# Kernel optimization log

Hardware: AMD Instinct MI355X
Metric: run time of the kernel (lower is better)

Reference implementation:

```python
import jax, jax.numpy as jnp
import numpy as np
import math

D_MODEL = 1024
NUM_HEADS = 16
D_K = D_MODEL // NUM_HEADS
B, S = 2, 2048


def setup_inputs() -> dict:
    key = jax.random.key(0)
    ks = jax.random.split(key, 11)
    scale = 1.0 / math.sqrt(D_MODEL)
    inp = {
        "query": jax.random.normal(ks[0], (B, S, D_MODEL), jnp.float32),
        "key": jax.random.normal(ks[1], (B, S, D_MODEL), jnp.float32),
        "value": jax.random.normal(ks[2], (B, S, D_MODEL), jnp.float32),
        "Wq": jax.random.normal(ks[3], (D_MODEL, D_MODEL), jnp.float32) * scale,
        "bq": jnp.zeros((D_MODEL,), jnp.float32),
        "Wk": jax.random.normal(ks[4], (D_MODEL, D_MODEL), jnp.float32) * scale,
        "bk": jnp.zeros((D_MODEL,), jnp.float32),
        "Wv": jax.random.normal(ks[5], (D_MODEL, D_MODEL), jnp.float32) * scale,
        "bv": jnp.zeros((D_MODEL,), jnp.float32),
        "Wo": jax.random.normal(ks[6], (D_MODEL, D_MODEL), jnp.float32) * scale,
        "bo": jnp.zeros((D_MODEL,), jnp.float32),
    }
    return inp


def reference(query, key, value, Wq, bq, Wk, bk, Wv, bv, Wo, bo):
    b, s, _ = query.shape
    # QKV projections (torch Linear: x @ W.T + b)
    Q = query @ Wq.T + bq
    K = key @ Wk.T + bk
    V = value @ Wv.T + bv
    # [b, h, s, d_k]
    Q = Q.reshape(b, s, NUM_HEADS, D_K).transpose(0, 2, 1, 3)
    K = K.reshape(b, s, NUM_HEADS, D_K).transpose(0, 2, 1, 3)
    V = V.reshape(b, s, NUM_HEADS, D_K).transpose(0, 2, 1, 3)
    score = jnp.einsum("bhqd,bhkd->bhqk", Q, K) / math.sqrt(D_K)
    attn = jax.nn.softmax(score, axis=-1)
    out = jnp.einsum("bhqk,bhkd->bhqd", attn, V)
    out = out.transpose(0, 2, 1, 3).reshape(b, s, D_MODEL)
    return out @ Wo.T + bo
```

## Files before the change

kernel.cpp:

```cpp
#include <hip/hip_runtime.h>

#define NHEADS 16
#define SEQ    2048
#define BATCH  2
#define DMODEL 1024
#define MTOT   4096

typedef __attribute__((ext_vector_type(8)))  short short8;
typedef __attribute__((ext_vector_type(4)))  float f32x4;
typedef __attribute__((ext_vector_type(16))) float f32x16;

__device__ __forceinline__ unsigned short f32_to_bf16_rn(float x) {
  unsigned int u = __float_as_uint(x);
  u += 0x7fffu + ((u >> 16) & 1u);
  return (unsigned short)(u >> 16);
}

__device__ __forceinline__ unsigned cvt_pk_bf16(float lo, float hi_) {
  unsigned r;
  asm("v_cvt_pk_bf16_f32 %0, %1, %2" : "=v"(r) : "v"(lo), "v"(hi_));
  return r;
}

__device__ __forceinline__ void permlane32_swap(unsigned &a, unsigned &b) {
  asm("v_permlane32_swap_b32 %0, %1" : "+v"(a), "+v"(b));
}

__device__ __forceinline__ void async16(void* lds, const void* g) {
  __builtin_amdgcn_global_load_lds((const __attribute__((address_space(1))) unsigned int*)g,
                                   (__attribute__((address_space(3))) unsigned int*)lds, 16, 0, 0);
}

__global__ void cvt_w_kernel(const float* __restrict__ w0, const float* __restrict__ w1,
                             const float* __restrict__ w2, const float* __restrict__ w3,
                             unsigned short* __restrict__ obase)
{
  const int which = blockIdx.y;
  const float* src = which==0 ? w0 : which==1 ? w1 : which==2 ? w2 : w3;
  const int i = (blockIdx.x*256 + threadIdx.x)*8;
  const float4 v0 = *(const float4*)(src + i);
  const float4 v1 = *(const float4*)(src + i + 4);
  union { unsigned short u[8]; uint4 v; } r;
  r.u[0] = f32_to_bf16_rn(v0.x); r.u[1] = f32_to_bf16_rn(v0.y);
  r.u[2] = f32_to_bf16_rn(v0.z); r.u[3] = f32_to_bf16_rn(v0.w);
  r.u[4] = f32_to_bf16_rn(v1.x); r.u[5] = f32_to_bf16_rn(v1.y);
  r.u[6] = f32_to_bf16_rn(v1.z); r.u[7] = f32_to_bf16_rn(v1.w);
  *(uint4*)(obase + (size_t)which*1048576 + i) = r.v;
}

template<int BM>
__device__ __forceinline__ void gemm_core(const unsigned short* __restrict__ A,
                                          const unsigned short* __restrict__ W,
                                          unsigned short* sA, unsigned short* sB,
                                          int m0, int n0, f32x4 (&acc)[BM/32][4])
{
  constexpr int MI = BM/32;
  const int t = threadIdx.x;
  const int lane = t & 63;
  const int wv = t >> 6;
  const int wm = wv >> 1, wn = wv & 1;
  const int lr = lane & 15, lk = lane >> 4;

  for (int kt = 0; kt < DMODEL/64; ++kt) {
    #pragma unroll
    for (int g = 0; g < MI; ++g) {
      const int o  = g*4096 + t*16;
      const int so = o ^ (((o >> 7) & 7) << 4);
      const int row = so >> 7, colE = (so & 127) >> 1;
      async16((char*)sA + o, A + (size_t)(m0 + row)*DMODEL + kt*64 + colE);
    }
    #pragma unroll
    for (int g = 0; g < 4; ++g) {
      const int o  = g*4096 + t*16;
      const int so = o ^ (((o >> 7) & 7) << 4);
      const int row = so >> 7, colE = (so & 127) >> 1;
      async16((char*)sB + o, W + (size_t)(n0 + row)*DMODEL + kt*64 + colE);
    }
    __syncthreads();
    #pragma unroll
    for (int ks = 0; ks < 2; ++ks) {
      short8 af[MI], bf[4];
      #pragma unroll
      for (int mi = 0; mi < MI; ++mi) {
        const int row = wm*(BM/2) + mi*16 + lr;
        const int sl  = (ks*4 + lk) ^ (row & 7);
        af[mi] = *(const short8*)(sA + row*64 + sl*8);
      }
      #pragma unroll
      for (int ni = 0; ni < 4; ++ni) {
        const int row = wn*64 + ni*16 + lr;
        const int sl  = (ks*4 + lk) ^ (row & 7);
        bf[ni] = *(const short8*)(sB + row*64 + sl*8);
      }
      #pragma unroll
      for (int mi = 0; mi < MI; ++mi)
        #pragma unroll
        for (int ni = 0; ni < 4; ++ni)
          acc[mi][ni] = __builtin_amdgcn_mfma_f32_16x16x32_bf16(af[mi], bf[ni], acc[mi][ni], 0, 0, 0);
    }
    __syncthreads();
  }
}

__global__ __launch_bounds__(256, 3)
void qkv_gemm_kernel(const float* __restrict__ Xq, const float* __restrict__ Xk,
                     const float* __restrict__ Xv,
                     const unsigned short* __restrict__ Wq, const unsigned short* __restrict__ Wk,
                     const unsigned short* __restrict__ Wv,
                     const float* __restrict__ bq, const float* __restrict__ bk,
                     const float* __restrict__ bv,
                     unsigned short* __restrict__ Qp, unsigned short* __restrict__ Kp,
                     unsigned short* __restrict__ Vtp)
{
  constexpr int MI = 4;
  constexpr int NK = DMODEL/64;
  __shared__ __align__(16) unsigned short smem[24576];
  unsigned short* sA = smem;

  const int m0   = blockIdx.x * 128;
  const int nabs = blockIdx.y * 128;
  const int wsel = nabs >> 10;
  const int n0   = nabs & 1023;
  const float* A          = wsel==0 ? Xq : wsel==1 ? Xk : Xv;
  const unsigned short* W = wsel==0 ? Wq : wsel==1 ? Wk : Wv;
  const float* bias       = wsel==0 ? bq : wsel==1 ? bk : bv;

  const int t = threadIdx.x, lane = t & 63, wvx = t >> 6;
  const int wm = wvx >> 1, wn = wvx & 1;
  const int lr = lane & 15, lk = lane >> 4;

  int aRow[MI], aCol[MI], aO[MI];
  #pragma unroll
  for (int g = 0; g < MI; ++g) {
    const int o  = g*4096 + t*16;
    const int so = o ^ (((o >> 7) & 7) << 4);
    aO[g] = o; aRow[g] = so >> 7; aCol[g] = (so & 127) >> 1;
  }

  f32x4 acc[MI][4];
  #pragma unroll
  for (int mi = 0; mi < MI; ++mi)
    #pragma unroll
    for (int ni = 0; ni < 4; ++ni)
      acc[mi][ni] = {0.f, 0.f, 0.f, 0.f};

  float4 aLo[MI], aHi[MI];
  #pragma unroll
  for (int g = 0; g < MI; ++g) {
    const float* s = A + (size_t)(m0 + aRow[g])*DMODEL + aCol[g];
    aLo[g] = *(const float4*)(s);
    aHi[g] = *(const float4*)(s + 4);
  }
  #pragma unroll
  for (int g = 0; g < 4; ++g)
    async16((char*)smem + 16384 + aO[g], W + (size_t)(n0 + aRow[g])*DMODEL + aCol[g]);

  for (int kt = 0; kt < NK; ++kt) {
    asm volatile("s_waitcnt vmcnt(0)" ::: "memory");
    #pragma unroll
    for (int g = 0; g < MI; ++g) {
      union { uint4 v; unsigned u[4]; } r;
      r.u[0] = cvt_pk_bf16(aLo[g].x, aLo[g].y);
      r.u[1] = cvt_pk_bf16(aLo[g].z, aLo[g].w);
      r.u[2] = cvt_pk_bf16(aHi[g].x, aHi[g].y);
      r.u[3] = cvt_pk_bf16(aHi[g].z, aHi[g].w);
      *(uint4*)((char*)sA + aO[g]) = r.v;
    }
    asm volatile("s_waitcnt lgkmcnt(0)" ::: "memory");
    __builtin_amdgcn_s_barrier();
    if (kt + 1 < NK) {
      #pragma unroll
      for (int g = 0; g < MI; ++g) {
        const float* s = A + (size_t)(m0 + aRow[g])*DMODEL + (kt + 1)*64 + aCol[g];
        aLo[g] = *(const float4*)(s);
        aHi[g] = *(const float4*)(s + 4);
      }
      const int nb = 16384 + ((kt + 1) & 1)*8192*2;
      #pragma unroll
      for (int g = 0; g < 4; ++g)
        async16((char*)smem + nb + aO[g], W + (size_t)(n0 + aRow[g])*DMODEL + (kt + 1)*64 + aCol[g]);
    }
    const unsigned short* sB = smem + 8192 + (kt & 1)*8192;
    #pragma unroll
    for (int ks = 0; ks < 2; ++ks) {
      short8 af[MI], bf[4];
      #pragma unroll
      for (int mi = 0; mi < MI; ++mi) {
        const int row = wm*64 + mi*16 + lr;
        const int sl  = (ks*4 + lk) ^ (row & 7);
        af[mi] = *(const short8*)(sA + row*64 + sl*8);
      }
      #pragma unroll
      for (int ni = 0; ni < 4; ++ni) {
        const int row = wn*64 + ni*16 + lr;
        const int sl  = (ks*4 + lk) ^ (row & 7);
        bf[ni] = *(const short8*)(sB + row*64 + sl*8);
      }
      #pragma unroll
      for (int mi = 0; mi < MI; ++mi)
        #pragma unroll
        for (int ni = 0; ni < 4; ++ni)
          acc[mi][ni] = __builtin_amdgcn_mfma_f32_16x16x32_bf16(af[mi], bf[ni], acc[mi][ni], 0, 0, 0);
    }
    __builtin_amdgcn_s_barrier();
  }
  __syncthreads();

  if (wsel == 2) {
    #pragma unroll
    for (int ni = 0; ni < 4; ++ni) {
      const float badd = bias[n0 + wn*64 + ni*16 + lr];
      #pragma unroll
      for (int mi = 0; mi < MI; ++mi)
        #pragma unroll
        for (int r = 0; r < 4; ++r) {
          const int ml = wm*64 + mi*16 + lk*4 + r;
          smem[(wn*64 + ni*16 + lr)*132 + ml] = f32_to_bf16_rn(acc[mi][ni][r] + badd);
        }
    }
    __syncthreads();
    const int bb = m0 >> 11, s0 = m0 & 2047;
    const int jr = (t & 15)*8, nr = t >> 4;
    #pragma unroll
    for (int pass = 0; pass < 8; ++pass) {
      const int n  = pass*16 + nr;
      const int nn = n0 + n, hh = nn >> 6, d = nn & 63;
      const short8 v = *(const short8*)(smem + n*132 + jr);
      *(short8*)(Vtp + (((size_t)bb*NHEADS + hh)*64 + d)*SEQ + s0 + jr) = v;
    }
  } else {
    unsigned short* dst = wsel==0 ? Qp : Kp;
    const float qscale = (wsel == 0) ? 0.125f * 1.4426950408889634f : 1.0f;
    #pragma unroll
    for (int ni = 0; ni < 4; ++ni) {
      const int nn = n0 + wn*64 + ni*16 + lr;
      const float badd = bias[nn];
      const int hh = nn >> 6, d = nn & 63;
      #pragma unroll
      for (int mi = 0; mi < MI; ++mi) {
        #pragma unroll
        for (int r = 0; r < 4; ++r) {
          const int m = m0 + wm*64 + mi*16 + lk*4 + r;
          const int bb = m >> 11, s = m & 2047;
          const float v = (acc[mi][ni][r] + badd) * qscale;
          dst[(((size_t)bb*NHEADS + hh)*SEQ + s)*64 + d] = f32_to_bf16_rn(v);
        }
      }
    }
  }
}

__global__ __launch_bounds__(256, 2)
void attn_kernel(const unsigned short* __restrict__ Qp, const unsigned short* __restrict__ Kp,
                 const unsigned short* __restrict__ Vtp, unsigned short* __restrict__ Op)
{
  __shared__ __align__(16) unsigned short sm[16384];
  constexpr int NT = SEQ/64;

  const int t = threadIdx.x, lane = t & 63, w = t >> 6;
  const int lq = lane & 31, hi = lane >> 5;
  const int f   = blockIdx.x;
  const int wid = (f & 7)*64 + (f >> 3);
  const int qt = wid & 15, h = (wid >> 4) & 15, b = wid >> 8;

  const size_t bh = (size_t)b*NHEADS + h;
  const unsigned short* Qh = Qp  + bh*SEQ*64;
  const unsigned short* Kh = Kp  + bh*SEQ*64;
  const unsigned short* Vh = Vtp + bh*64*SEQ;
  const int q0 = qt*128 + w*32;

  short8 qf[4];
  #pragma unroll
  for (int ks = 0; ks < 4; ++ks)
    qf[ks] = *(const short8*)(Qh + (size_t)(q0 + lq)*64 + ks*16 + hi*8);

  f32x16 z16;
  #pragma unroll
  for (int r = 0; r < 16; ++r) z16[r] = 0.f;

  const unsigned short* srcp0;
  size_t sstride;
  if (w < 2) { srcp0 = Kh + (size_t)(w*32 + lq)*64 + hi*8;       sstride = 64*64; }
  else       { srcp0 = Vh + (size_t)((w-2)*32 + lq)*2048 + hi*8; sstride = 64;    }

  #pragma unroll
  for (int i = 0; i < 4; ++i)
    async16((char*)sm + w*4096 + i*1024, srcp0 + i*16);

  f32x16 o[2];
  float lsa[4] = {0.f, 0.f, 0.f, 0.f};
  #pragma unroll
  for (int d = 0; d < 2; ++d)
    #pragma unroll
    for (int r = 0; r < 16; ++r) o[d][r] = 0.f;

  for (int kt = 0; kt < NT; ++kt) {
    {
      const unsigned short* sp = srcp0 + (size_t)((kt + 1) & (NT - 1))*sstride;
      const int nb = ((kt + 1) & 1) * 16384;
      #pragma unroll
      for (int i = 0; i < 4; ++i)
        async16((char*)sm + nb + w*4096 + i*1024, sp + i*16);
    }
    asm volatile("s_waitcnt vmcnt(4)" ::: "memory");
    __builtin_amdgcn_s_barrier();

    const unsigned short* base  = sm + (kt & 1)*8192;
    const unsigned short* vbase = base + 4096;

    f32x16 st[2];
    #pragma unroll
    for (int sub = 0; sub < 2; ++sub) {
      #pragma unroll
      for (int ks = 0; ks < 4; ++ks) {
        const short8 kf = *(const short8*)(base + (sub*4 + ks)*512 + lane*8);
        if (ks == 0)
          st[sub] = __builtin_amdgcn_mfma_f32_32x32x16_bf16(kf, qf[0], z16, 0, 0, 0);
        else
          st[sub] = __builtin_amdgcn_mfma_f32_32x32x16_bf16(kf, qf[ks], st[sub], 0, 0, 0);
      }
    }

    unsigned pw[2][8];
    #pragma unroll
    for (int sub = 0; sub < 2; ++sub) {
      #pragma unroll
      for (int r = 0; r < 16; ++r) {
        const float p = __builtin_amdgcn_exp2f(st[sub][r]);
        st[sub][r] = p;
        lsa[r & 3] += p;
      }
      unsigned x0 = cvt_pk_bf16(st[sub][0],  st[sub][1]);
      unsigned x1 = cvt_pk_bf16(st[sub][2],  st[sub][3]);
      unsigned y0 = cvt_pk_bf16(st[sub][4],  st[sub][5]);
      unsigned y1 = cvt_pk_bf16(st[sub][6],  st[sub][7]);
      permlane32_swap(x0, y0);
      permlane32_swap(x1, y1);
      pw[sub][0] = x0; pw[sub][1] = x1; pw[sub][2] = y0; pw[sub][3] = y1;
      unsigned z0 = cvt_pk_bf16(st[sub][8],  st[sub][9]);
      unsigned z1 = cvt_pk_bf16(st[sub][10], st[sub][11]);
      unsigned w0 = cvt_pk_bf16(st[sub][12], st[sub][13]);
      unsigned w1 = cvt_pk_bf16(st[sub][14], st[sub][15]);
      permlane32_swap(z0, w0);
      permlane32_swap(z1, w1);
      pw[sub][4] = z0; pw[sub][5] = z1; pw[sub][6] = w0; pw[sub][7] = w1;
    }

    #pragma unroll
    for (int sub = 0; sub < 2; ++sub) {
      const short8 v00 = *(const short8*)(vbase + (0*4 + 2*sub    )*512 + lane*8);
      const short8 v01 = *(const short8*)(vbase + (0*4 + 2*sub + 1)*512 + lane*8);
      const short8 v10 = *(const short8*)(vbase + (1*4 + 2*sub    )*512 + lane*8);
      const short8 v11 = *(const short8*)(vbase + (1*4 + 2*sub + 1)*512 + lane*8);
      union { unsigned u[4]; short8 s; } pA, pB;
      pA.u[0] = pw[sub][0]; pA.u[1] = pw[sub][1]; pA.u[2] = pw[sub][2]; pA.u[3] = pw[sub][3];
      pB.u[0] = pw[sub][4]; pB.u[1] = pw[sub][5]; pB.u[2] = pw[sub][6]; pB.u[3] = pw[sub][7];
      o[0] = __builtin_amdgcn_mfma_f32_32x32x16_bf16(v00, pA.s, o[0], 0, 0, 0);
      o[1] = __builtin_amdgcn_mfma_f32_32x32x16_bf16(v10, pA.s, o[1], 0, 0, 0);
      o[0] = __builtin_amdgcn_mfma_f32_32x32x16_bf16(v01, pB.s, o[0], 0, 0, 0);
      o[1] = __builtin_amdgcn_mfma_f32_32x32x16_bf16(v11, pB.s, o[1], 0, 0, 0);
    }
    asm volatile("" ::: "memory");
    __builtin_amdgcn_s_barrier();
  }

  float lsum = (lsa[0] + lsa[1]) + (lsa[2] + lsa[3]);
  lsum += __shfl_xor(lsum, 32);
  const float inv = __builtin_amdgcn_rcpf(lsum);
  unsigned short* orow = Op + ((size_t)b*SEQ + q0 + lq)*DMODEL + h*64;
  #pragma unroll
  for (int dblk = 0; dblk < 2; ++dblk)
    #pragma unroll
    for (int g = 0; g < 4; ++g) {
      union { unsigned short us[4]; uint2 v; } pk;
      #pragma unroll
      for (int r = 0; r < 4; ++r) pk.us[r] = f32_to_bf16_rn(o[dblk][g*4 + r] * inv);
      *(uint2*)(orow + dblk*32 + g*8 + hi*4) = pk.v;
    }
}

__global__ __launch_bounds__(256, 2)
void oproj_gemm_kernel(const unsigned short* __restrict__ Oin, const unsigned short* __restrict__ Wo,
                       const float* __restrict__ bo, float* __restrict__ out)
{
  constexpr int BM = 64;
  constexpr int MI = BM/32;
  __shared__ __align__(16) unsigned short sA[BM*64];
  __shared__ __align__(16) unsigned short sB[128*64];
  const int m0 = blockIdx.x * BM;
  const int n0 = blockIdx.y * 128;

  f32x4 acc[MI][4];
  #pragma unroll
  for (int mi = 0; mi < MI; ++mi)
    #pragma unroll
    for (int ni = 0; ni < 4; ++ni)
      acc[mi][ni] = {0.f,0.f,0.f,0.f};

  gemm_core<BM>(Oin, Wo, sA, sB, m0, n0, acc);

  const int t = threadIdx.x, lane = t & 63, wvx = t >> 6;
  const int wm = wvx >> 1, wn = wvx & 1;
  const int lr = lane & 15, lk = lane >> 4;

  #pragma unroll
  for (int ni = 0; ni < 4; ++ni) {
    const int nn = n0 + wn*64 + ni*16 + lr;
    const float badd = bo[nn];
    #pragma unroll
    for (int mi = 0; mi < MI; ++mi)
      #pragma unroll
      for (int r = 0; r < 4; ++r) {
        const int m = m0 + wm*(BM/2) + mi*16 + lk*4 + r;
        out[(size_t)m*DMODEL + nn] = acc[mi][ni][r] + badd;
      }
  }
}

extern "C" void kernel_launch(void* const* d_in, const int* in_sizes, int n_in,
                              void* d_out, int out_size, void* d_ws, size_t ws_size,
                              hipStream_t stream) {
  const float* query = (const float*)d_in[0];
  const float* key   = (const float*)d_in[1];
  const float* value = (const float*)d_in[2];
  const float* Wq    = (const float*)d_in[3];
  const float* bq    = (const float*)d_in[4];
  const float* Wk    = (const float*)d_in[5];
  const float* bk    = (const float*)d_in[6];
  const float* Wv    = (const float*)d_in[7];
  const float* bv    = (const float*)d_in[8];
  const float* Wo    = (const float*)d_in[9];
  const float* bo    = (const float*)d_in[10];

  const size_t NX = (size_t)MTOT*DMODEL;
  const size_t NW = (size_t)DMODEL*DMODEL;
  unsigned short* w   = (unsigned short*)d_ws;
  unsigned short* Wqp = w + 3*NX;
  unsigned short* Wkp = Wqp + NW;
  unsigned short* Wvp = Wkp + NW;
  unsigned short* Wop = Wvp + NW;
  unsigned short* Qp  = Wop + NW;
  unsigned short* Kp  = Qp  + NX;
  unsigned short* Vtp = Kp  + NX;
  unsigned short* Opb = Vtp + NX;

  cvt_w_kernel<<<dim3(512, 4), 256, 0, stream>>>(Wq, Wk, Wv, Wo, Wqp);
  qkv_gemm_kernel<<<dim3(32, 24), 256, 0, stream>>>(
      query, key, value, Wqp, Wkp, Wvp, bq, bk, bv, Qp, Kp, Vtp);
  attn_kernel<<<dim3(512), 256, 0, stream>>>(Qp, Kp, Vtp, Opb);
  oproj_gemm_kernel<<<dim3(64, 8), 256, 0, stream>>>(Opb, Wop, bo, (float*)d_out);
}
```

Baseline: 105.0 us.

## Deepen A-operand register prefetch to two stages with partial vmcnt waits

```diff
diff --git a/kernel.cpp b/kernel.cpp
--- a/kernel.cpp
+++ b/kernel.cpp
@@ -144,41 +144,52 @@
     for (int ni = 0; ni < 4; ++ni)
       acc[mi][ni] = {0.f, 0.f, 0.f, 0.f};
 
-  float4 aLo[MI], aHi[MI];
+  float4 aLoA[MI], aHiA[MI], aLoB[MI], aHiB[MI];
+
   #pragma unroll
   for (int g = 0; g < MI; ++g) {
     const float* s = A + (size_t)(m0 + aRow[g])*DMODEL + aCol[g];
-    aLo[g] = *(const float4*)(s);
-    aHi[g] = *(const float4*)(s + 4);
+    aLoA[g] = *(const float4*)(s);
+    aHiA[g] = *(const float4*)(s + 4);
   }
   #pragma unroll
   for (int g = 0; g < 4; ++g)
     async16((char*)smem + 16384 + aO[g], W + (size_t)(n0 + aRow[g])*DMODEL + aCol[g]);
-
-  for (int kt = 0; kt < NK; ++kt) {
-    asm volatile("s_waitcnt vmcnt(0)" ::: "memory");
+  #pragma unroll
+  for (int g = 0; g < MI; ++g) {
+    const float* s = A + (size_t)(m0 + aRow[g])*DMODEL + 64 + aCol[g];
+    aLoB[g] = *(const float4*)(s);
+    aHiB[g] = *(const float4*)(s + 4);
+  }
+
+  auto body = [&](int kt, float4 (&lo)[MI], float4 (&hi)[MI]) {
+    {
+      const int bkt = (kt + 1) & (NK - 1);
+      const int nb  = 16384 + ((kt + 1) & 1)*16384;
+      #pragma unroll
+      for (int g = 0; g < 4; ++g)
+        async16((char*)smem + nb + aO[g], W + (size_t)(n0 + aRow[g])*DMODEL + bkt*64 + aCol[g]);
+    }
+    asm volatile("s_waitcnt vmcnt(12)" ::: "memory");
     #pragma unroll
     for (int g = 0; g < MI; ++g) {
       union { uint4 v; unsigned u[4]; } r;
-      r.u[0] = cvt_pk_bf16(aLo[g].x, aLo[g].y);
-      r.u[1] = cvt_pk_bf16(aLo[g].z, aLo[g].w);
-      r.u[2] = cvt_pk_bf16(aHi[g].x, aHi[g].y);
-      r.u[3] = cvt_pk_bf16(aHi[g].z, aHi[g].w);
+      r.u[0] = cvt_pk_bf16(lo[g].x, lo[g].y);
+      r.u[1] = cvt_pk_bf16(lo[g].z, lo[g].w);
+      r.u[2] = cvt_pk_bf16(hi[g].x, hi[g].y);
+      r.u[3] = cvt_pk_bf16(hi[g].z, hi[g].w);
       *(uint4*)((char*)sA + aO[g]) = r.v;
     }
     asm volatile("s_waitcnt lgkmcnt(0)" ::: "memory");
     __builtin_amdgcn_s_barrier();
-    if (kt + 1 < NK) {
+    {
+      const int akt = (kt + 2) & (NK - 1);
       #pragma unroll
       for (int g = 0; g < MI; ++g) {
-        const float* s = A + (size_t)(m0 + aRow[g])*DMODEL + (kt + 1)*64 + aCol[g];
-        aLo[g] = *(const float4*)(s);
-        aHi[g] = *(const float4*)(s + 4);
-      }
-      const int nb = 16384 + ((kt + 1) & 1)*8192*2;
-      #pragma unroll
-      for (int g = 0; g < 4; ++g)
-        async16((char*)smem + nb + aO[g], W + (size_t)(n0 + aRow[g])*DMODEL + (kt + 1)*64 + aCol[g]);
+        const float* s = A + (size_t)(m0 + aRow[g])*DMODEL + akt*64 + aCol[g];
+        lo[g] = *(const float4*)(s);
+        hi[g] = *(const float4*)(s + 4);
+      }
     }
     const unsigned short* sB = smem + 8192 + (kt & 1)*8192;
     #pragma unroll
@@ -203,6 +214,11 @@
           acc[mi][ni] = __builtin_amdgcn_mfma_f32_16x16x32_bf16(af[mi], bf[ni], acc[mi][ni], 0, 0, 0);
     }
     __builtin_amdgcn_s_barrier();
+  };
+
+  for (int kt = 0; kt < NK; kt += 2) {
+    body(kt,     aLoA, aHiA);
+    body(kt + 1, aLoB, aHiB);
   }
   __syncthreads();
 
```

New measurement: 112.7 us. +7.3%, slower.

## Double attention KV tile to 128 keys and pin scheduling with sched barriers

Applied to the files above, without the earlier changes.

```diff
diff --git a/kernel.cpp b/kernel.cpp
--- a/kernel.cpp
+++ b/kernel.cpp
@@ -168,6 +168,7 @@
     }
     asm volatile("s_waitcnt lgkmcnt(0)" ::: "memory");
     __builtin_amdgcn_s_barrier();
+    __builtin_amdgcn_sched_barrier(0);
     if (kt + 1 < NK) {
       #pragma unroll
       for (int g = 0; g < MI; ++g) {
@@ -202,7 +203,9 @@
         for (int ni = 0; ni < 4; ++ni)
           acc[mi][ni] = __builtin_amdgcn_mfma_f32_16x16x32_bf16(af[mi], bf[ni], acc[mi][ni], 0, 0, 0);
     }
+    asm volatile("" ::: "memory");
     __builtin_amdgcn_s_barrier();
+    __builtin_amdgcn_sched_barrier(0);
   }
   __syncthreads();
 
@@ -254,8 +257,8 @@
 void attn_kernel(const unsigned short* __restrict__ Qp, const unsigned short* __restrict__ Kp,
                  const unsigned short* __restrict__ Vtp, unsigned short* __restrict__ Op)
 {
-  __shared__ __align__(16) unsigned short sm[16384];
-  constexpr int NT = SEQ/64;
+  __shared__ __align__(16) unsigned short sm[32768];
+  constexpr int NT = SEQ/128;
 
   const int t = threadIdx.x, lane = t & 63, w = t >> 6;
   const int lq = lane & 31, hi = lane >> 5;
@@ -280,12 +283,22 @@
 
   const unsigned short* srcp0;
   size_t sstride;
-  if (w < 2) { srcp0 = Kh + (size_t)(w*32 + lq)*64 + hi*8;       sstride = 64*64; }
-  else       { srcp0 = Vh + (size_t)((w-2)*32 + lq)*2048 + hi*8; sstride = 64;    }
-
-  #pragma unroll
-  for (int i = 0; i < 4; ++i)
-    async16((char*)sm + w*4096 + i*1024, srcp0 + i*16);
+  int offi[8];
+  if (w < 2) {
+    srcp0 = Kh + (size_t)(w*64 + lq)*64 + hi*8;
+    sstride = 128*64;
+    #pragma unroll
+    for (int i = 0; i < 8; ++i) offi[i] = (i >> 2)*2048 + (i & 3)*16;
+  } else {
+    srcp0 = Vh + (size_t)((w - 2)*32 + lq)*2048 + hi*8;
+    sstride = 128;
+    #pragma unroll
+    for (int i = 0; i < 8; ++i) offi[i] = i*16;
+  }
+
+  #pragma unroll
+  for (int i = 0; i < 8; ++i)
+    async16((char*)sm + w*8192 + i*1024, srcp0 + offi[i]);
 
   f32x16 o[2];
   float lsa[4] = {0.f, 0.f, 0.f, 0.f};
@@ -297,64 +310,57 @@
   for (int kt = 0; kt < NT; ++kt) {
     {
       const unsigned short* sp = srcp0 + (size_t)((kt + 1) & (NT - 1))*sstride;
-      const int nb = ((kt + 1) & 1) * 16384;
-      #pragma unroll
-      for (int i = 0; i < 4; ++i)
-        async16((char*)sm + nb + w*4096 + i*1024, sp + i*16);
-    }
-    asm volatile("s_waitcnt vmcnt(4)" ::: "memory");
+      const int nb = ((kt + 1) & 1) * 32768;
+      #pragma unroll
+      for (int i = 0; i < 8; ++i)
+        async16((char*)sm + nb + w*8192 + i*1024, sp + offi[i]);
+    }
+    asm volatile("s_waitcnt vmcnt(8)" ::: "memory");
     __builtin_amdgcn_s_barrier();
-
-    const unsigned short* base  = sm + (kt & 1)*8192;
-    const unsigned short* vbase = base + 4096;
-
-    f32x16 st[2];
-    #pragma unroll
-    for (int sub = 0; sub < 2; ++sub) {
+    __builtin_amdgcn_sched_barrier(0);
+    asm volatile("" ::: "memory");
+
+    const unsigned short* kb = sm + (kt & 1)*16384;
+    const unsigned short* vb = kb + 8192;
+
+    #pragma unroll
+    for (int sub = 0; sub < 4; ++sub) {
+      f32x16 st;
       #pragma unroll
       for (int ks = 0; ks < 4; ++ks) {
-        const short8 kf = *(const short8*)(base + (sub*4 + ks)*512 + lane*8);
+        const short8 kf = *(const short8*)(kb + (sub*4 + ks)*512 + lane*8);
         if (ks == 0)
-          st[sub] = __builtin_amdgcn_mfma_f32_32x32x16_bf16(kf, qf[0], z16, 0, 0, 0);
+          st = __builtin_amdgcn_mfma_f32_32x32x16_bf16(kf, qf[0], z16, 0, 0, 0);
         else
-          st[sub] = __builtin_amdgcn_mfma_f32_32x32x16_bf16(kf, qf[ks], st[sub], 0, 0, 0);
-      }
-    }
-
-    unsigned pw[2][8];
-    #pragma unroll
-    for (int sub = 0; sub < 2; ++sub) {
+          st = __builtin_amdgcn_mfma_f32_32x32x16_bf16(kf, qf[ks], st, 0, 0, 0);
+      }
       #pragma unroll
       for (int r = 0; r < 16; ++r) {
-        const float p = __builtin_amdgcn_exp2f(st[sub][r]);
-        st[sub][r] = p;
+        const float p = __builtin_amdgcn_exp2f(st[r]);
+        st[r] = p;
         lsa[r & 3] += p;
       }
-      unsigned x0 = cvt_pk_bf16(st[sub][0],  st[sub][1]);
-      unsigned x1 = cvt_pk_bf16(st[sub][2],  st[sub][3]);
-      unsigned y0 = cvt_pk_bf16(st[sub][4],  st[sub][5]);
-      unsigned y1 = cvt_pk_bf16(st[sub][6],  st[sub][7]);
-      permlane32_swap(x0, y0);
-      permlane32_swap(x1, y1);
-      pw[sub][0] = x0; pw[sub][1] = x1; pw[sub][2] = y0; pw[sub][3] = y1;
-      unsigned z0 = cvt_pk_bf16(st[sub][8],  st[sub][9]);
-      unsigned z1 = cvt_pk_bf16(st[sub][10], st[sub][11]);
-      unsigned w0 = cvt_pk_bf16(st[sub][12], st[sub][13]);
-      unsigned w1 = cvt_pk_bf16(st[sub][14], st[sub][15]);
-      permlane32_swap(z0, w0);
-      permlane32_swap(z1, w1);
-      pw[sub][4] = z0; pw[sub][5] = z1; pw[sub][6] = w0; pw[sub][7] = w1;
-    }
-
-    #pragma unroll
-    for (int sub = 0; sub < 2; ++sub) {
-      const short8 v00 = *(const short8*)(vbase + (0*4 + 2*sub    )*512 + lane*8);
-      const short8 v01 = *(const short8*)(vbase + (0*4 + 2*sub + 1)*512 + lane*8);
-      const short8 v10 = *(const short8*)(vbase + (1*4 + 2*sub    )*512 + lane*8);
-      const short8 v11 = *(const short8*)(vbase + (1*4 + 2*sub + 1)*512 + lane*8);
       union { unsigned u[4]; short8 s; } pA, pB;
-      pA.u[0] = pw[sub][0]; pA.u[1] = pw[sub][1]; pA.u[2] = pw[sub][2]; pA.u[3] = pw[sub][3];
-      pB.u[0] = pw[sub][4]; pB.u[1] = pw[sub][5]; pB.u[2] = pw[sub][6]; pB.u[3] = pw[sub][7];
+      {
+        unsigned x0 = cvt_pk_bf16(st[0],  st[1]);
+        unsigned x1 = cvt_pk_bf16(st[2],  st[3]);
+        unsigned y0 = cvt_pk_bf16(st[4],  st[5]);
+        unsigned y1 = cvt_pk_bf16(st[6],  st[7]);
+        permlane32_swap(x0, y0);
+        permlane32_swap(x1, y1);
+        pA.u[0] = x0; pA.u[1] = x1; pA.u[2] = y0; pA.u[3] = y1;
+        unsigned z0 = cvt_pk_bf16(st[8],  st[9]);
+        unsigned z1 = cvt_pk_bf16(st[10], st[11]);
+        unsigned w0 = cvt_pk_bf16(st[12], st[13]);
+        unsigned w1 = cvt_pk_bf16(st[14], st[15]);
+        permlane32_swap(z0, w0);
+        permlane32_swap(z1, w1);
+        pB.u[0] = z0; pB.u[1] = z1; pB.u[2] = w0; pB.u[3] = w1;
+      }
+      const short8 v00 = *(const short8*)(vb + (0*8 + 2*sub    )*512 + lane*8);
+      const short8 v01 = *(const short8*)(vb + (0*8 + 2*sub + 1)*512 + lane*8);
+      const short8 v10 = *(const short8*)(vb + (1*8 + 2*sub    )*512 + lane*8);
+      const short8 v11 = *(const short8*)(vb + (1*8 + 2*sub + 1)*512 + lane*8);
       o[0] = __builtin_amdgcn_mfma_f32_32x32x16_bf16(v00, pA.s, o[0], 0, 0, 0);
       o[1] = __builtin_amdgcn_mfma_f32_32x32x16_bf16(v10, pA.s, o[1], 0, 0, 0);
       o[0] = __builtin_amdgcn_mfma_f32_32x32x16_bf16(v01, pB.s, o[0], 0, 0, 0);
@@ -362,7 +368,9 @@
     }
     asm volatile("" ::: "memory");
     __builtin_amdgcn_s_barrier();
-  }
+    __builtin_amdgcn_sched_barrier(0);
+  }
+  asm volatile("s_waitcnt vmcnt(0)" ::: "memory");
 
   float lsum = (lsa[0] + lsa[1]) + (lsa[2] + lsa[3]);
   lsum += __shfl_xor(lsum, 32);
```

Result: slower. 107.2 us (+2.1%).

## Enlarge QKV GEMM block tile to 256x128 with 512 threads

Applied to the files above, without the earlier changes.

```diff
diff --git a/kernel.cpp b/kernel.cpp
--- a/kernel.cpp
+++ b/kernel.cpp
@@ -102,7 +102,7 @@
   }
 }
 
-__global__ __launch_bounds__(256, 3)
+__global__ __launch_bounds__(512, 2)
 void qkv_gemm_kernel(const float* __restrict__ Xq, const float* __restrict__ Xk,
                      const float* __restrict__ Xv,
                      const unsigned short* __restrict__ Wq, const unsigned short* __restrict__ Wk,
@@ -114,10 +114,9 @@
 {
   constexpr int MI = 4;
   constexpr int NK = DMODEL/64;
-  __shared__ __align__(16) unsigned short smem[24576];
-  unsigned short* sA = smem;
-
-  const int m0   = blockIdx.x * 128;
+  __shared__ __align__(16) unsigned short smem[33792];
+
+  const int m0   = blockIdx.x * 256;
   const int nabs = blockIdx.y * 128;
   const int wsel = nabs >> 10;
   const int n0   = nabs & 1023;
@@ -129,13 +128,20 @@
   const int wm = wvx >> 1, wn = wvx & 1;
   const int lr = lane & 15, lk = lane >> 4;
 
-  int aRow[MI], aCol[MI], aO[MI];
-  #pragma unroll
-  for (int g = 0; g < MI; ++g) {
-    const int o  = g*4096 + t*16;
+  int aRow[4], aCol[4], aO[4];
+  #pragma unroll
+  for (int g = 0; g < 4; ++g) {
+    const int o  = g*8192 + t*16;
     const int so = o ^ (((o >> 7) & 7) << 4);
     aO[g] = o; aRow[g] = so >> 7; aCol[g] = (so & 127) >> 1;
   }
+  int bRow[2], bCol[2], bO[2];
+  #pragma unroll
+  for (int g = 0; g < 2; ++g) {
+    const int o  = g*8192 + t*16;
+    const int so = o ^ (((o >> 7) & 7) << 4);
+    bO[g] = o; bRow[g] = so >> 7; bCol[g] = (so & 127) >> 1;
+  }
 
   f32x4 acc[MI][4];
   #pragma unroll
@@ -144,43 +150,43 @@
     for (int ni = 0; ni < 4; ++ni)
       acc[mi][ni] = {0.f, 0.f, 0.f, 0.f};
 
-  float4 aLo[MI], aHi[MI];
-  #pragma unroll
-  for (int g = 0; g < MI; ++g) {
+  float4 aLo[4], aHi[4];
+  #pragma unroll
+  for (int g = 0; g < 4; ++g) {
     const float* s = A + (size_t)(m0 + aRow[g])*DMODEL + aCol[g];
     aLo[g] = *(const float4*)(s);
     aHi[g] = *(const float4*)(s + 4);
   }
   #pragma unroll
-  for (int g = 0; g < 4; ++g)
-    async16((char*)smem + 16384 + aO[g], W + (size_t)(n0 + aRow[g])*DMODEL + aCol[g]);
+  for (int g = 0; g < 2; ++g)
+    async16((char*)smem + 32768 + bO[g], W + (size_t)(n0 + bRow[g])*DMODEL + bCol[g]);
 
   for (int kt = 0; kt < NK; ++kt) {
     asm volatile("s_waitcnt vmcnt(0)" ::: "memory");
     #pragma unroll
-    for (int g = 0; g < MI; ++g) {
+    for (int g = 0; g < 4; ++g) {
       union { uint4 v; unsigned u[4]; } r;
       r.u[0] = cvt_pk_bf16(aLo[g].x, aLo[g].y);
       r.u[1] = cvt_pk_bf16(aLo[g].z, aLo[g].w);
       r.u[2] = cvt_pk_bf16(aHi[g].x, aHi[g].y);
       r.u[3] = cvt_pk_bf16(aHi[g].z, aHi[g].w);
-      *(uint4*)((char*)sA + aO[g]) = r.v;
+      *(uint4*)((char*)smem + aO[g]) = r.v;
     }
     asm volatile("s_waitcnt lgkmcnt(0)" ::: "memory");
     __builtin_amdgcn_s_barrier();
     if (kt + 1 < NK) {
       #pragma unroll
-      for (int g = 0; g < MI; ++g) {
+      for (int g = 0; g < 4; ++g) {
         const float* s = A + (size_t)(m0 + aRow[g])*DMODEL + (kt + 1)*64 + aCol[g];
         aLo[g] = *(const float4*)(s);
         aHi[g] = *(const float4*)(s + 4);
       }
-      const int nb = 16384 + ((kt + 1) & 1)*8192*2;
-      #pragma unroll
-      for (int g = 0; g < 4; ++g)
-        async16((char*)smem + nb + aO[g], W + (size_t)(n0 + aRow[g])*DMODEL + (kt + 1)*64 + aCol[g]);
-    }
-    const unsigned short* sB = smem + 8192 + (kt & 1)*8192;
+      const int nb = 32768 + ((kt + 1) & 1)*16384;
+      #pragma unroll
+      for (int g = 0; g < 2; ++g)
+        async16((char*)smem + nb + bO[g], W + (size_t)(n0 + bRow[g])*DMODEL + (kt + 1)*64 + bCol[g]);
+    }
+    const unsigned short* sBu = smem + 16384 + (kt & 1)*8192;
     #pragma unroll
     for (int ks = 0; ks < 2; ++ks) {
       short8 af[MI], bf[4];
@@ -188,13 +194,13 @@
       for (int mi = 0; mi < MI; ++mi) {
         const int row = wm*64 + mi*16 + lr;
         const int sl  = (ks*4 + lk) ^ (row & 7);
-        af[mi] = *(const short8*)(sA + row*64 + sl*8);
+        af[mi] = *(const short8*)(smem + row*64 + sl*8);
       }
       #pragma unroll
       for (int ni = 0; ni < 4; ++ni) {
         const int row = wn*64 + ni*16 + lr;
         const int sl  = (ks*4 + lk) ^ (row & 7);
-        bf[ni] = *(const short8*)(sB + row*64 + sl*8);
+        bf[ni] = *(const short8*)(sBu + row*64 + sl*8);
       }
       #pragma unroll
       for (int mi = 0; mi < MI; ++mi)
@@ -215,17 +221,17 @@
         #pragma unroll
         for (int r = 0; r < 4; ++r) {
           const int ml = wm*64 + mi*16 + lk*4 + r;
-          smem[(wn*64 + ni*16 + lr)*132 + ml] = f32_to_bf16_rn(acc[mi][ni][r] + badd);
+          smem[(wn*64 + ni*16 + lr)*264 + ml] = f32_to_bf16_rn(acc[mi][ni][r] + badd);
         }
     }
     __syncthreads();
     const int bb = m0 >> 11, s0 = m0 & 2047;
-    const int jr = (t & 15)*8, nr = t >> 4;
+    const int jr = (t & 31)*8, nr = t >> 5;
     #pragma unroll
     for (int pass = 0; pass < 8; ++pass) {
       const int n  = pass*16 + nr;
       const int nn = n0 + n, hh = nn >> 6, d = nn & 63;
-      const short8 v = *(const short8*)(smem + n*132 + jr);
+      const short8 v = *(const short8*)(smem + n*264 + jr);
       *(short8*)(Vtp + (((size_t)bb*NHEADS + hh)*64 + d)*SEQ + s0 + jr) = v;
     }
   } else {
@@ -445,7 +451,7 @@
   unsigned short* Opb = Vtp + NX;
 
   cvt_w_kernel<<<dim3(512, 4), 256, 0, stream>>>(Wq, Wk, Wv, Wo, Wqp);
-  qkv_gemm_kernel<<<dim3(32, 24), 256, 0, stream>>>(
+  qkv_gemm_kernel<<<dim3(16, 24), 512, 0, stream>>>(
       query, key, value, Wqp, Wkp, Wvp, bq, bk, bv, Qp, Kp, Vtp);
   attn_kernel<<<dim3(512), 256, 0, stream>>>(Qp, Kp, Vtp, Opb);
   oproj_gemm_kernel<<<dim3(64, 8), 256, 0, stream>>>(Opb, Wop, bo, (float*)d_out);
```

Result: slower. 118.7 us (+13.0%).
